# Optimization experiments

Measured on AMD Instinct MI355X. Metric: run time of the kernel, lower is better.

The kernel has to match this reference:

```python
import jax, jax.numpy as jnp
import numpy as np

N = 8192
E = 262144
IN_SELF = 512
IN_AGG = 512
OUT = 256  # out_channels; hidden = 2*OUT = 512


def _glorot(key, shape, scale=0.05):
    return jax.random.normal(key, shape, dtype=jnp.float32) * scale


def setup_inputs() -> dict:
    key = jax.random.key(0)
    ks = jax.random.split(key, 16)
    x_self = jax.random.normal(ks[0], (N, IN_SELF), dtype=jnp.float32)
    x_neighbor = jax.random.normal(ks[1], (N, IN_AGG), dtype=jnp.float32)
    edge_index = jax.random.randint(ks[2], (2, E), 0, N, dtype=jnp.int64)
    H = 2 * OUT
    return {
        "x_self": x_self,
        "x_neighbor": x_neighbor,
        "edge_index": edge_index,
        # linear_in_self: IN_SELF -> 2*OUT
        "w_in_self": _glorot(ks[3], (IN_SELF, H)),
        "b_in_self": jnp.zeros((H,), jnp.float32),
        # linear_out_self: IN_SELF + 2*OUT -> OUT
        "w_out_self": _glorot(ks[4], (IN_SELF + H, OUT)),
        "b_out_self": jnp.zeros((OUT,), jnp.float32),
        # gcn1: IN_SELF -> 2*OUT
        "gw1": _glorot(ks[5], (IN_SELF, H)),
        "gb1": jnp.zeros((H,), jnp.float32),
        # gcn2: 2*OUT -> OUT
        "gw2": _glorot(ks[6], (H, OUT)),
        "gb2": jnp.zeros((OUT,), jnp.float32),
        # linear_out: IN_AGG + OUT -> OUT
        "w_out": _glorot(ks[7], (IN_AGG + OUT, OUT)),
        "b_out": jnp.zeros((OUT,), jnp.float32),
    }


def _gcn_norm(edge_index, n):
    # PyG GCNConv default: add self loops, symmetric deg^-1/2 normalization.
    loop = jnp.arange(n, dtype=edge_index.dtype)
    src = jnp.concatenate([edge_index[0], loop])
    dst = jnp.concatenate([edge_index[1], loop])
    deg = jax.ops.segment_sum(jnp.ones_like(dst, dtype=jnp.float32), dst, num_segments=n)
    dinv = jnp.where(deg > 0, jax.lax.rsqrt(deg), 0.0)
    norm = dinv[src] * dinv[dst]  # [E+N]
    return src, dst, norm


def _gcn(x, w, b, src, dst, norm, n):
    h = x @ w                                   # [N, out]
    msg = h[src] * norm[:, None]                # gather + scale
    agg = jax.ops.segment_sum(msg, dst, num_segments=n)
    return agg + b


def reference(x_self, x_neighbor, edge_index,
              w_in_self, b_in_self, w_out_self, b_out_self,
              gw1, gb1, gw2, gb2, w_out, b_out):
    n = x_self.shape[0]
    src, dst, norm = _gcn_norm(edge_index, n)
    # linear branch
    l1 = jax.nn.relu(x_self @ w_in_self + b_in_self)
    l1 = jnp.concatenate([x_self, l1], axis=1) @ w_out_self + b_out_self
    # GCN branch
    g1 = _gcn(x_self, gw1, gb1, src, dst, norm, n)
    g2 = _gcn(g1, gw2, gb2, src, dst, norm, n)
    x2 = jnp.concatenate([x_neighbor, g2], axis=1) @ w_out + b_out
    # concat latent, dense inner-product decode
    z = jnp.concatenate([l1, x2], axis=1)       # [N, 2*OUT]
    return jax.nn.sigmoid(z @ z.T)              # [N, N]
```

## Files before the change

kernel.cpp:

```cpp
#include <hip/hip_runtime.h>
#include <cstdint>
#include <cstddef>

#define NNODE 8192
#define NEDGE 262144

typedef __attribute__((ext_vector_type(8))) short bf16x8;
typedef __attribute__((ext_vector_type(4))) float f32x4;

__device__ __forceinline__ unsigned short f2bf_rn(float x) {
    unsigned u = __float_as_uint(x);
    u = (u + 0x7FFFu + ((u >> 16) & 1u)) >> 16;
    return (unsigned short)u;
}
__device__ __forceinline__ float bf2f(unsigned short h) {
    return __uint_as_float(((unsigned)h) << 16);
}

__device__ __forceinline__ void gload16(const char* gp, char* lp) {
    __builtin_amdgcn_global_load_lds((const __attribute__((address_space(1))) void*)gp,
                                     (__attribute__((address_space(3))) void*)lp, 16, 0, 0);
}


__global__ void k_zero_int(int* p, int n) {
    int i = blockIdx.x * blockDim.x + threadIdx.x;
    if (i < n) p[i] = 0;
}

__global__ void k_count(const int* __restrict__ dst, int* __restrict__ cnt, int n) {
    int i = blockIdx.x * blockDim.x + threadIdx.x;
    if (i < n) atomicAdd(&cnt[dst[i]], 1);
}

__global__ __launch_bounds__(256) void k_scan(const int* __restrict__ cnt,
                                              int* __restrict__ row_start,
                                              int* __restrict__ cursor,
                                              float* __restrict__ dinv) {
    __shared__ int part[256];
    const int tid = threadIdx.x;
    const int PER = NNODE / 256;
    const int base = tid * PER;
    int loc[PER];
    int sum = 0;
#pragma unroll
    for (int i = 0; i < PER; ++i) { loc[i] = cnt[base + i]; sum += loc[i]; }
    part[tid] = sum;
    __syncthreads();
    if (tid == 0) {
        int r = 0;
        for (int i = 0; i < 256; ++i) { int t = part[i]; part[i] = r; r += t; }
    }
    __syncthreads();
    int run = part[tid];
#pragma unroll
    for (int i = 0; i < PER; ++i) {
        row_start[base + i] = run;
        cursor[base + i] = run;
        dinv[base + i] = rsqrtf((float)loc[i] + 1.0f);
        run += loc[i];
    }
    if (tid == 255) row_start[NNODE] = run;
}

__global__ void k_fill_csr2(const int* __restrict__ src, const int* __restrict__ dst,
                            int* __restrict__ cursor, const float* __restrict__ dinv,
                            int* __restrict__ slist, float* __restrict__ wlist, int n) {
    int e = blockIdx.x * blockDim.x + threadIdx.x;
    if (e < n) {
        int d = dst[e];
        int s = src[e];
        int pos = atomicAdd(&cursor[d], 1);
        slist[pos] = s;
        wlist[pos] = dinv[s] * dinv[d];
    }
}

__device__ __forceinline__ void split_wt_tile(const float* __restrict__ W, int K, int N,
                                              int k0, int n0,
                                              unsigned short* __restrict__ Oh,
                                              unsigned short* __restrict__ Ol,
                                              float (*t)[33]) {
    const int c = threadIdx.x & 31, r8 = threadIdx.x >> 5;
#pragma unroll
    for (int i = 0; i < 4; ++i) {
        int r = r8 + i * 8;
        t[r][c] = W[(size_t)(k0 + r) * N + n0 + c];
    }
    __syncthreads();
#pragma unroll
    for (int i = 0; i < 4; ++i) {
        int r = r8 + i * 8;
        float x = t[c][r];
        unsigned short h = f2bf_rn(x);
        Oh[(size_t)(n0 + r) * K + k0 + c] = h;
        Ol[(size_t)(n0 + r) * K + k0 + c] = f2bf_rn(x - bf2f(h));
    }
}

__global__ __launch_bounds__(256) void k_prep(
    const float* __restrict__ x_self, const float* __restrict__ x_neighbor,
    const float* __restrict__ w_in_self, const float* __restrict__ w_out_self,
    const float* __restrict__ w_out, const float* __restrict__ gw1,
    const float* __restrict__ gw2, const float* __restrict__ gb1,
    unsigned short* __restrict__ xsh, unsigned short* __restrict__ xsl,
    unsigned short* __restrict__ xnh, unsigned short* __restrict__ xnl,
    unsigned short* __restrict__ wAt_h, unsigned short* __restrict__ wAt_l,
    unsigned short* __restrict__ wost_h, unsigned short* __restrict__ wost_l,
    unsigned short* __restrict__ wot_h, unsigned short* __restrict__ wot_l,
    float* __restrict__ bc) {
    __shared__ float t[32][33];
    const int b = blockIdx.x;
    const int tid = threadIdx.x;
    if (b < 8192) {
        const float* src = (b < 4096) ? x_self : x_neighbor;
        unsigned short* oh = (b < 4096) ? xsh : xnh;
        unsigned short* ol = (b < 4096) ? xsl : xnl;
        const int i = (b & 4095) * 256 + tid;
        float4 v = ((const float4*)src)[i];
        float x[4] = {v.x, v.y, v.z, v.w};
        unsigned short h[4], l[4];
#pragma unroll
        for (int j = 0; j < 4; ++j) {
            h[j] = f2bf_rn(x[j]);
            l[j] = f2bf_rn(x[j] - bf2f(h[j]));
        }
        ((ushort4*)oh)[i] = make_ushort4(h[0], h[1], h[2], h[3]);
        ((ushort4*)ol)[i] = make_ushort4(l[0], l[1], l[2], l[3]);
    } else if (b < 8448) {
        const int b2 = b - 8192;
        split_wt_tile(w_in_self, 512, 512, (b2 & 15) * 32, (b2 >> 4) * 32, wAt_h, wAt_l, t);
    } else if (b < 8576) {
        const int b3 = b - 8448;
        const int k0 = (b3 & 15) * 32, n0 = (b3 >> 4) * 32;
        const int nloc = tid & 31, kg = tid >> 5;
        float a[4] = {0.f, 0.f, 0.f, 0.f};
        for (int c = 0; c < 512; ++c) {
            float g2v = gw2[(size_t)c * 256 + n0 + nloc];
#pragma unroll
            for (int i = 0; i < 4; ++i)
                a[i] += gw1[(size_t)(k0 + kg * 4 + i) * 512 + c] * g2v;
        }
#pragma unroll
        for (int i = 0; i < 4; ++i) {
            unsigned short hh = f2bf_rn(a[i]);
            wAt_h[(size_t)(512 + n0 + nloc) * 512 + k0 + kg * 4 + i] = hh;
            wAt_l[(size_t)(512 + n0 + nloc) * 512 + k0 + kg * 4 + i] = f2bf_rn(a[i] - bf2f(hh));
        }
    } else if (b < 8832) {
        const int b4 = b - 8576;
        split_wt_tile(w_out_self, 1024, 256, (b4 & 31) * 32, (b4 >> 5) * 32, wost_h, wost_l, t);
    } else if (b < 9024) {
        const int b5 = b - 8832;
        split_wt_tile(w_out, 768, 256, (b5 % 24) * 32, (b5 / 24) * 32, wot_h, wot_l, t);
    } else {
        float a = 0.0f;
        for (int c = 0; c < 512; ++c) a += gb1[c] * gw2[(size_t)c * 256 + tid];
        bc[tid] = a;
    }
}

__device__ __forceinline__ void stage_g(char* buf,
                                        const char* aH, const char* aL, size_t strA,
                                        const char* bH, const char* bL, size_t strB,
                                        int rloc, int w) {
#pragma unroll
    for (int i = 0; i < 2; ++i) {
        const size_t r = (size_t)(rloc + i * 64);
        char* lp = buf + i * 4096 + w * 1024;
        gload16(aH + r * strA, lp);
        gload16(aL + r * strA, lp + 8192);
    }
    gload16(bH + (size_t)rloc * strB, buf + 16384 + w * 1024);
    gload16(bL + (size_t)rloc * strB, buf + 20480 + w * 1024);
}

__device__ __forceinline__ void core_2x4(const char* cur, int w, int sread, int lane,
                                         f32x4 acc[2][4]) {
    bf16x8 ah[2], al[2], bh[4], bl[4];
#pragma unroll
    for (int m = 0; m < 2; ++m) {
        const int row = w * 32 + m * 16 + (lane & 15);
        ah[m] = *(const bf16x8*)(cur + row * 64 + sread);
        al[m] = *(const bf16x8*)(cur + 8192 + row * 64 + sread);
    }
#pragma unroll
    for (int n = 0; n < 4; ++n) {
        const int row = n * 16 + (lane & 15);
        bh[n] = *(const bf16x8*)(cur + 16384 + row * 64 + sread);
        bl[n] = *(const bf16x8*)(cur + 20480 + row * 64 + sread);
    }
#pragma unroll
    for (int m = 0; m < 2; ++m)
#pragma unroll
        for (int n = 0; n < 4; ++n) {
            acc[m][n] = __builtin_amdgcn_mfma_f32_16x16x32_bf16(ah[m], bh[n], acc[m][n], 0, 0, 0);
            acc[m][n] = __builtin_amdgcn_mfma_f32_16x16x32_bf16(ah[m], bl[n], acc[m][n], 0, 0, 0);
            acc[m][n] = __builtin_amdgcn_mfma_f32_16x16x32_bf16(al[m], bh[n], acc[m][n], 0, 0, 0);
        }
}

__global__ __launch_bounds__(256) void k_gemm128_A(
    const unsigned short* __restrict__ xsh, const unsigned short* __restrict__ xsl,
    const unsigned short* __restrict__ wAt_h, const unsigned short* __restrict__ wAt_l,
    const float* __restrict__ bias,
    unsigned short* __restrict__ l1h, unsigned short* __restrict__ l1l,
    float* __restrict__ hc) {
    __shared__ __align__(16) char smem[49152];
    const int tid = threadIdx.x, lane = tid & 63, w = tid >> 6;
    const int bm = blockIdx.y * 128, bn = blockIdx.x * 64;
    const int rloc = w * 16 + (lane >> 2);
    const int swz_src = ((lane & 3) ^ ((lane >> 3) & 3)) * 16;
    const int sread = ((lane >> 4) ^ ((lane >> 1) & 3)) * 16;
    const char* Ah = (const char*)xsh + (size_t)bm * 1024 + swz_src;
    const char* Al = (const char*)xsl + (size_t)bm * 1024 + swz_src;
    const char* Bh = (const char*)wAt_h + (size_t)bn * 1024 + swz_src;
    const char* Bl = (const char*)wAt_l + (size_t)bn * 1024 + swz_src;

    f32x4 acc[2][4] = {};
    stage_g(smem, Ah, Al, 1024, Bh, Bl, 1024, rloc, w);
    __syncthreads();
    for (int ks = 0; ks < 16; ++ks) {
        char* cur = smem + (ks & 1) * 24576;
        if (ks < 15) {
            const int kb = (ks + 1) * 64;
            stage_g(smem + ((ks + 1) & 1) * 24576, Ah + kb, Al + kb, 1024,
                    Bh + kb, Bl + kb, 1024, rloc, w);
        }
        core_2x4(cur, w, sread, lane, acc);
        __syncthreads();
    }

    const int rj = (lane >> 4) * 4, cc = lane & 15;
#pragma unroll
    for (int m = 0; m < 2; ++m) {
#pragma unroll
        for (int n = 0; n < 4; ++n) {
            const int col = bn + n * 16 + cc;
#pragma unroll
            for (int j = 0; j < 4; ++j) {
                const int row = bm + w * 32 + m * 16 + rj + j;
                float x = acc[m][n][j];
                if (col < 512) {
                    x += bias[col];
                    x = fmaxf(x, 0.0f);
                    unsigned short h = f2bf_rn(x);
                    l1h[(size_t)row * 512 + col] = h;
                    l1l[(size_t)row * 512 + col] = f2bf_rn(x - bf2f(h));
                } else {
                    hc[(size_t)row * 256 + (col - 512)] = x;
                }
            }
        }
    }
}

__global__ __launch_bounds__(256) void k_gemm128_Z(
    const unsigned short* __restrict__ xsh, const unsigned short* __restrict__ xsl,
    const unsigned short* __restrict__ l1h, const unsigned short* __restrict__ l1l,
    const unsigned short* __restrict__ xnh, const unsigned short* __restrict__ xnl,
    const unsigned short* __restrict__ g2h, const unsigned short* __restrict__ g2l,
    const unsigned short* __restrict__ wost_h, const unsigned short* __restrict__ wost_l,
    const unsigned short* __restrict__ wot_h, const unsigned short* __restrict__ wot_l,
    const float* __restrict__ b_out_self, const float* __restrict__ b_out,
    unsigned short* __restrict__ zhi, unsigned short* __restrict__ zlo) {
    __shared__ __align__(16) char smem[49152];
    const int half = blockIdx.x >> 2;
    const int bn = (blockIdx.x & 3) * 64;
    const int tid = threadIdx.x, lane = tid & 63, w = tid >> 6;
    const int bm = blockIdx.y * 128;
    const int rloc = w * 16 + (lane >> 2);
    const int swz_src = ((lane & 3) ^ ((lane >> 3) & 3)) * 16;
    const int sread = ((lane >> 4) ^ ((lane >> 1) & 3)) * 16;

    const unsigned short *A1h, *A1l, *A2h, *A2l, *Wh, *Wl;
    const float* bias;
    int Ktot;
    size_t strA2, strB;
    if (half == 0) {
        A1h = xsh; A1l = xsl; A2h = l1h; A2l = l1l; strA2 = 1024;
        Wh = wost_h; Wl = wost_l; strB = 2048; Ktot = 1024; bias = b_out_self;
    } else {
        A1h = xnh; A1l = xnl; A2h = g2h; A2l = g2l; strA2 = 512;
        Wh = wot_h; Wl = wot_l; strB = 1536; Ktot = 768; bias = b_out;
    }
    const int nsteps = Ktot / 32;
    const char* Bh = (const char*)Wh + (size_t)bn * strB + swz_src;
    const char* Bl = (const char*)Wl + (size_t)bn * strB + swz_src;

    auto asrc = [&](int k0, const char*& sh, const char*& sl, size_t& st) {
        if (k0 < 512) {
            sh = (const char*)A1h + (size_t)bm * 1024 + (size_t)k0 * 2 + swz_src;
            sl = (const char*)A1l + (size_t)bm * 1024 + (size_t)k0 * 2 + swz_src;
            st = 1024;
        } else {
            sh = (const char*)A2h + (size_t)bm * strA2 + (size_t)(k0 - 512) * 2 + swz_src;
            sl = (const char*)A2l + (size_t)bm * strA2 + (size_t)(k0 - 512) * 2 + swz_src;
            st = strA2;
        }
    };

    f32x4 acc[2][4] = {};
    {
        const char *sh, *sl; size_t st;
        asrc(0, sh, sl, st);
        stage_g(smem, sh, sl, st, Bh, Bl, strB, rloc, w);
    }
    __syncthreads();
    for (int ks = 0; ks < nsteps; ++ks) {
        char* cur = smem + (ks & 1) * 24576;
        if (ks + 1 < nsteps) {
            const char *sh, *sl; size_t st;
            asrc((ks + 1) * 32, sh, sl, st);
            stage_g(smem + ((ks + 1) & 1) * 24576, sh, sl, st,
                    Bh + (size_t)(ks + 1) * 64, Bl + (size_t)(ks + 1) * 64, strB, rloc, w);
        }
        core_2x4(cur, w, sread, lane, acc);
        __syncthreads();
    }

    const int rj = (lane >> 4) * 4, cc = lane & 15;
    const int zoff = half * 256;
#pragma unroll
    for (int m = 0; m < 2; ++m) {
#pragma unroll
        for (int n = 0; n < 4; ++n) {
            const int col = bn + n * 16 + cc;
            const float bv = bias[col];
#pragma unroll
            for (int j = 0; j < 4; ++j) {
                const int row = bm + w * 32 + m * 16 + rj + j;
                float x = acc[m][n][j] + bv;
                unsigned short h = f2bf_rn(x);
                zhi[(size_t)row * 512 + zoff + col] = h;
                zlo[(size_t)row * 512 + zoff + col] = f2bf_rn(x - bf2f(h));
            }
        }
    }
}

template <int MODE>
__global__ __launch_bounds__(256) void k_agg2(
    const int* __restrict__ row_start, const int* __restrict__ slist,
    const float* __restrict__ wlist, const float* __restrict__ dinv,
    const float* __restrict__ h,
    const float* __restrict__ bc, const float* __restrict__ b2,
    float* __restrict__ outf,
    unsigned short* __restrict__ oh, unsigned short* __restrict__ ol) {
    const int n = blockIdx.x;
    const int c = threadIdx.x;
    const float di = dinv[n];
    float acc = di * di * h[(size_t)n * 256 + c];
    float sv = di * di;
    const int e0 = row_start[n], e1 = row_start[n + 1];
    int j = e0;
    for (; j + 8 <= e1; j += 8) {
        int ss[8];
        float ww[8], vv[8];
#pragma unroll
        for (int u = 0; u < 8; ++u) { ss[u] = slist[j + u]; ww[u] = wlist[j + u]; }
#pragma unroll
        for (int u = 0; u < 8; ++u) vv[u] = h[(size_t)ss[u] * 256 + c];
#pragma unroll
        for (int u = 0; u < 8; ++u) {
            acc += ww[u] * vv[u];
            if (MODE) sv += ww[u];
        }
    }
    for (; j < e1; ++j) {
        const float wv = wlist[j];
        acc += wv * h[(size_t)slist[j] * 256 + c];
        if (MODE) sv += wv;
    }
    if (MODE == 0) {
        outf[(size_t)n * 256 + c] = acc;
    } else {
        float x = acc + sv * bc[c] + b2[c];
        unsigned short hb = f2bf_rn(x);
        oh[(size_t)n * 256 + c] = hb;
        ol[(size_t)n * 256 + c] = f2bf_rn(x - bf2f(hb));
    }
}

__device__ __forceinline__ void zzt_stage(char* buf, const char* s0, const char* s1,
                                          const char* s2, const char* s3,
                                          int rloc, int swz_src, int w, int kbyte) {
    const char* srcs[4] = {s0, s1, s2, s3};
#pragma unroll
    for (int tile = 0; tile < 4; ++tile) {
#pragma unroll
        for (int i = 0; i < 2; ++i) {
            const char* gp = srcs[tile] + (size_t)(rloc + i * 64) * 1024 + kbyte + swz_src;
            char* lp = buf + tile * 8192 + i * 4096 + w * 1024;
            gload16(gp, lp);
        }
    }
}

__global__ __launch_bounds__(256) void k_zzt_mfma(const unsigned short* __restrict__ zhi,
                                                  const unsigned short* __restrict__ zlo,
                                                  float* __restrict__ out) {
    __shared__ __align__(16) char smem[65536];
    const int tid = threadIdx.x;
    const int lane = tid & 63;
    const int w = tid >> 6;
    const int wr = w >> 1, wc = w & 1;

    const int t = blockIdx.x;
    int bi = (int)((sqrtf(8.0f * (float)t + 1.0f) - 1.0f) * 0.5f);
    while ((bi + 1) * (bi + 2) / 2 <= t) ++bi;
    while (bi * (bi + 1) / 2 > t) --bi;
    const int bj = t - bi * (bi + 1) / 2;

    const char* s0 = (const char*)zhi + (size_t)(bi * 128) * 1024;
    const char* s1 = (const char*)zlo + (size_t)(bi * 128) * 1024;
    const char* s2 = (const char*)zhi + (size_t)(bj * 128) * 1024;
    const char* s3 = (const char*)zlo + (size_t)(bj * 128) * 1024;

    const int rloc = w * 16 + (lane >> 2);
    const int swz_src = ((lane & 3) ^ ((lane >> 3) & 3)) * 16;
    const int sread = ((lane >> 4) ^ ((lane >> 1) & 3)) * 16;

    f32x4 acc[4][4] = {};

    zzt_stage(smem, s0, s1, s2, s3, rloc, swz_src, w, 0);
    __syncthreads();

    for (int ks = 0; ks < 16; ++ks) {
        char* cur = smem + (ks & 1) * 32768;
        if (ks < 15)
            zzt_stage(smem + ((ks + 1) & 1) * 32768, s0, s1, s2, s3, rloc, swz_src, w,
                      (ks + 1) * 64);

        bf16x8 ah[4], al[4], bh[4], bl[4];
        const char* pa = cur + (wr * 64 + (lane & 15)) * 64 + sread;
        const char* pb = cur + 16384 + (wc * 64 + (lane & 15)) * 64 + sread;
#pragma unroll
        for (int m = 0; m < 4; ++m) {
            ah[m] = *(const bf16x8*)(pa + m * 1024);
            al[m] = *(const bf16x8*)(pa + 8192 + m * 1024);
        }
#pragma unroll
        for (int n = 0; n < 4; ++n) {
            bh[n] = *(const bf16x8*)(pb + n * 1024);
            bl[n] = *(const bf16x8*)(pb + 8192 + n * 1024);
        }
#pragma unroll
        for (int m = 0; m < 4; ++m)
#pragma unroll
            for (int n = 0; n < 4; ++n) {
                acc[m][n] = __builtin_amdgcn_mfma_f32_16x16x32_bf16(ah[m], bh[n], acc[m][n], 0, 0, 0);
                acc[m][n] = __builtin_amdgcn_mfma_f32_16x16x32_bf16(ah[m], bl[n], acc[m][n], 0, 0, 0);
                acc[m][n] = __builtin_amdgcn_mfma_f32_16x16x32_bf16(al[m], bh[n], acc[m][n], 0, 0, 0);
            }
        __syncthreads();
    }

    const int rj = (lane >> 4) * 4;
    const int cc = lane & 15;
#pragma unroll
    for (int m = 0; m < 4; ++m) {
#pragma unroll
        for (int n = 0; n < 4; ++n) {
            float s[4];
#pragma unroll
            for (int j = 0; j < 4; ++j)
                s[j] = 1.0f / (1.0f + __expf(-acc[m][n][j]));
            const int gr0 = bi * 128 + wr * 64 + m * 16 + rj;
            const int gc  = bj * 128 + wc * 64 + n * 16 + cc;
#pragma unroll
            for (int j = 0; j < 4; ++j)
                __builtin_nontemporal_store(s[j], out + (size_t)(gr0 + j) * NNODE + gc);
            if (bi != bj) {
                const int mr = bj * 128 + wc * 64 + n * 16 + cc;
                const int mc = bi * 128 + wr * 64 + m * 16 + rj;
                f32x4 v = {s[0], s[1], s[2], s[3]};
                __builtin_nontemporal_store(v, (f32x4*)(out + (size_t)mr * NNODE + mc));
            }
        }
    }
}

extern "C" void kernel_launch(void* const* d_in, const int* in_sizes, int n_in,
                              void* d_out, int out_size, void* d_ws, size_t ws_size,
                              hipStream_t stream) {
    const float* x_self     = (const float*)d_in[0];
    const float* x_neighbor = (const float*)d_in[1];
    const int*   ei         = (const int*)d_in[2];
    const float* w_in_self  = (const float*)d_in[3];
    const float* b_in_self  = (const float*)d_in[4];
    const float* w_out_self = (const float*)d_in[5];
    const float* b_out_self = (const float*)d_in[6];
    const float* gw1        = (const float*)d_in[7];
    const float* gb1        = (const float*)d_in[8];
    const float* gw2        = (const float*)d_in[9];
    const float* gb2        = (const float*)d_in[10];
    const float* w_out      = (const float*)d_in[11];
    const float* b_out      = (const float*)d_in[12];
    float* out = (float*)d_out;

    char* ws = (char*)d_ws;
    const size_t MB = 1024 * 1024;
    const size_t KB = 1024;
    int*   cnt       = (int*)(ws + 0);
    int*   row_start = (int*)(ws + 32 * KB);
    int*   cursor    = (int*)(ws + 96 * KB);
    float* dinv      = (float*)(ws + 128 * KB);
    float* bc        = (float*)(ws + 192 * KB);
    int*   slist     = (int*)(ws + 2 * MB);
    float* wlist     = (float*)(ws + 3 * MB);
    unsigned short* xsh = (unsigned short*)(ws + 4 * MB);
    unsigned short* xsl = (unsigned short*)(ws + 12 * MB);
    unsigned short* xnh = (unsigned short*)(ws + 20 * MB);
    unsigned short* xnl = (unsigned short*)(ws + 28 * MB);
    unsigned short* l1h = (unsigned short*)(ws + 36 * MB);
    unsigned short* l1l = (unsigned short*)(ws + 44 * MB);
    float*          hc  = (float*)(ws + 52 * MB);
    float*          t1  = (float*)(ws + 60 * MB);
    unsigned short* g2h = (unsigned short*)(ws + 68 * MB);
    unsigned short* g2l = (unsigned short*)(ws + 72 * MB);
    unsigned short* zhi = (unsigned short*)(ws + 76 * MB);
    unsigned short* zlo = (unsigned short*)(ws + 84 * MB);
    unsigned short* wAt_h = (unsigned short*)(ws + 92 * MB);
    unsigned short* wAt_l = (unsigned short*)(ws + 93 * MB);
    unsigned short* wost_h = (unsigned short*)(ws + 94 * MB);
    unsigned short* wost_l = (unsigned short*)(ws + 95 * MB);
    unsigned short* wot_h  = (unsigned short*)(ws + 96 * MB);
    unsigned short* wot_l  = (unsigned short*)(ws + 97 * MB);

    const int* srcA = ei;
    const int* dstA = ei + NEDGE;

    k_prep<<<9025, 256, 0, stream>>>(x_self, x_neighbor, w_in_self, w_out_self, w_out,
                                     gw1, gw2, gb1, xsh, xsl, xnh, xnl,
                                     wAt_h, wAt_l, wost_h, wost_l, wot_h, wot_l, bc);

    k_zero_int<<<NNODE / 256, 256, 0, stream>>>(cnt, NNODE);
    k_count<<<NEDGE / 256, 256, 0, stream>>>(dstA, cnt, NEDGE);
    k_scan<<<1, 256, 0, stream>>>(cnt, row_start, cursor, dinv);
    k_fill_csr2<<<NEDGE / 256, 256, 0, stream>>>(srcA, dstA, cursor, dinv, slist, wlist, NEDGE);

    k_gemm128_A<<<dim3(12, NNODE / 128), 256, 0, stream>>>(
        xsh, xsl, wAt_h, wAt_l, b_in_self, l1h, l1l, hc);

    k_agg2<0><<<NNODE, 256, 0, stream>>>(row_start, slist, wlist, dinv, hc,
                                         nullptr, nullptr, t1, nullptr, nullptr);
    k_agg2<1><<<NNODE, 256, 0, stream>>>(row_start, slist, wlist, dinv, t1,
                                         bc, gb2, nullptr, g2h, g2l);

    k_gemm128_Z<<<dim3(8, NNODE / 128), 256, 0, stream>>>(
        xsh, xsl, l1h, l1l, xnh, xnl, g2h, g2l,
        wost_h, wost_l, wot_h, wot_l, b_out_self, b_out, zhi, zlo);

    k_zzt_mfma<<<64 * 65 / 2, 256, 0, stream>>>(zhi, zlo, out);
}
```

Before: 390.0 us.

## Retile Z·Zᵀ decode to 256x256 blocks with deeper prefetch and fold count zeroing

The dense sigmoid(Z·Zᵀ) kernel now uses 256x256 output tiles over the upper triangle with 512 threads and 8 waves. Each wave computes 8x4 MFMA sub-tiles, doubling operand reuse per load. Staging is double-buffered two k-steps ahead with explicit vmcnt waits and raw barriers, MFMA phases get higher s_setprio, and the block index is remapped to interleave tiles. The separate zeroing kernel for degree counts is merged into the prep kernel as extra blocks, saving one launch. The cost is 128KB of LDS per block and higher register pressure, which limits occupancy.

```diff
diff --git a/kernel.cpp b/kernel.cpp
--- a/kernel.cpp
+++ b/kernel.cpp
@@ -22,11 +22,6 @@
                                      (__attribute__((address_space(3))) void*)lp, 16, 0, 0);
 }
 
-
-__global__ void k_zero_int(int* p, int n) {
-    int i = blockIdx.x * blockDim.x + threadIdx.x;
-    if (i < n) p[i] = 0;
-}
 
 __global__ void k_count(const int* __restrict__ dst, int* __restrict__ cnt, int n) {
     int i = blockIdx.x * blockDim.x + threadIdx.x;
@@ -108,7 +103,7 @@
     unsigned short* __restrict__ wAt_h, unsigned short* __restrict__ wAt_l,
     unsigned short* __restrict__ wost_h, unsigned short* __restrict__ wost_l,
     unsigned short* __restrict__ wot_h, unsigned short* __restrict__ wot_l,
-    float* __restrict__ bc) {
+    float* __restrict__ bc, int* __restrict__ cnt) {
     __shared__ float t[32][33];
     const int b = blockIdx.x;
     const int tid = threadIdx.x;
@@ -153,10 +148,12 @@
     } else if (b < 9024) {
         const int b5 = b - 8832;
         split_wt_tile(w_out, 768, 256, (b5 % 24) * 32, (b5 / 24) * 32, wot_h, wot_l, t);
-    } else {
+    } else if (b == 9024) {
         float a = 0.0f;
         for (int c = 0; c < 512; ++c) a += gb1[c] * gw2[(size_t)c * 256 + tid];
         bc[tid] = a;
+    } else {
+        cnt[(b - 9025) * 256 + tid] = 0;
     }
 }
 
@@ -382,98 +379,99 @@
     }
 }
 
-__device__ __forceinline__ void zzt_stage(char* buf, const char* s0, const char* s1,
-                                          const char* s2, const char* s3,
-                                          int rloc, int swz_src, int w, int kbyte) {
-    const char* srcs[4] = {s0, s1, s2, s3};
-#pragma unroll
-    for (int tile = 0; tile < 4; ++tile) {
-#pragma unroll
-        for (int i = 0; i < 2; ++i) {
-            const char* gp = srcs[tile] + (size_t)(rloc + i * 64) * 1024 + kbyte + swz_src;
-            char* lp = buf + tile * 8192 + i * 4096 + w * 1024;
-            gload16(gp, lp);
-        }
-    }
-}
-
-__global__ __launch_bounds__(256) void k_zzt_mfma(const unsigned short* __restrict__ zhi,
-                                                  const unsigned short* __restrict__ zlo,
-                                                  float* __restrict__ out) {
-    __shared__ __align__(16) char smem[65536];
+__global__ __launch_bounds__(512, 2) void k_zzt256(const unsigned short* __restrict__ zhi,
+                                                   const unsigned short* __restrict__ zlo,
+                                                   float* __restrict__ out) {
+    __shared__ __align__(16) char smem[131072];
     const int tid = threadIdx.x;
     const int lane = tid & 63;
     const int w = tid >> 6;
-    const int wr = w >> 1, wc = w & 1;
-
-    const int t = blockIdx.x;
+    const int wr = w >> 2, wc = w & 3;
+
+    const int t0 = blockIdx.x;
+    const int t = (t0 & 7) * 66 + (t0 >> 3);
     int bi = (int)((sqrtf(8.0f * (float)t + 1.0f) - 1.0f) * 0.5f);
     while ((bi + 1) * (bi + 2) / 2 <= t) ++bi;
     while (bi * (bi + 1) / 2 > t) --bi;
     const int bj = t - bi * (bi + 1) / 2;
 
-    const char* s0 = (const char*)zhi + (size_t)(bi * 128) * 1024;
-    const char* s1 = (const char*)zlo + (size_t)(bi * 128) * 1024;
-    const char* s2 = (const char*)zhi + (size_t)(bj * 128) * 1024;
-    const char* s3 = (const char*)zlo + (size_t)(bj * 128) * 1024;
-
-    const int rloc = w * 16 + (lane >> 2);
+    const char* pnl[4];
+    pnl[0] = (const char*)zhi + (size_t)(bi * 256) * 1024;
+    pnl[1] = (const char*)zlo + (size_t)(bi * 256) * 1024;
+    pnl[2] = (const char*)zhi + (size_t)(bj * 256) * 1024;
+    pnl[3] = (const char*)zlo + (size_t)(bj * 256) * 1024;
+
     const int swz_src = ((lane & 3) ^ ((lane >> 3) & 3)) * 16;
     const int sread = ((lane >> 4) ^ ((lane >> 1) & 3)) * 16;
 
-    f32x4 acc[4][4] = {};
-
-    zzt_stage(smem, s0, s1, s2, s3, rloc, swz_src, w, 0);
-    __syncthreads();
-
-    for (int ks = 0; ks < 16; ++ks) {
-        char* cur = smem + (ks & 1) * 32768;
-        if (ks < 15)
-            zzt_stage(smem + ((ks + 1) & 1) * 32768, s0, s1, s2, s3, rloc, swz_src, w,
-                      (ks + 1) * 64);
-
-        bf16x8 ah[4], al[4], bh[4], bl[4];
-        const char* pa = cur + (wr * 64 + (lane & 15)) * 64 + sread;
-        const char* pb = cur + 16384 + (wc * 64 + (lane & 15)) * 64 + sread;
-#pragma unroll
-        for (int m = 0; m < 4; ++m) {
-            ah[m] = *(const bf16x8*)(pa + m * 1024);
-            al[m] = *(const bf16x8*)(pa + 8192 + m * 1024);
-        }
+    auto STAGE = [&](int buf, int kt) {
+        const int kb = kt * 64;
+        char* base = smem + buf * 65536;
+#pragma unroll
+        for (int jj = 0; jj < 8; ++jj) {
+            const int c = w * 8 + jj;
+            const int q = c >> 4, ci = c & 15;
+            const char* gp = pnl[q] + (size_t)(ci * 16 + (lane >> 2)) * 1024 + kb + swz_src;
+            gload16(gp, base + q * 16384 + ci * 1024);
+        }
+    };
+
+    f32x4 acc[8][4] = {};
+
+    STAGE(0, 0);
+    STAGE(1, 1);
+
+    for (int kt = 0; kt < 16; ++kt) {
+        if (kt < 15) asm volatile("s_waitcnt vmcnt(8)" ::: "memory");
+        else         asm volatile("s_waitcnt vmcnt(0)" ::: "memory");
+        __builtin_amdgcn_s_barrier();
+        __builtin_amdgcn_sched_barrier(0);
+        const char* cur = smem + (kt & 1) * 65536;
+
+        bf16x8 bh[4], bl[4];
 #pragma unroll
         for (int n = 0; n < 4; ++n) {
-            bh[n] = *(const bf16x8*)(pb + n * 1024);
-            bl[n] = *(const bf16x8*)(pb + 8192 + n * 1024);
-        }
-#pragma unroll
-        for (int m = 0; m < 4; ++m)
+            const int row = wc * 64 + n * 16 + (lane & 15);
+            bh[n] = *(const bf16x8*)(cur + 32768 + row * 64 + sread);
+            bl[n] = *(const bf16x8*)(cur + 49152 + row * 64 + sread);
+        }
+#pragma unroll
+        for (int m = 0; m < 8; ++m) {
+            const int row = wr * 128 + m * 16 + (lane & 15);
+            bf16x8 ah = *(const bf16x8*)(cur + row * 64 + sread);
+            bf16x8 al = *(const bf16x8*)(cur + 16384 + row * 64 + sread);
+            __builtin_amdgcn_s_setprio(1);
 #pragma unroll
             for (int n = 0; n < 4; ++n) {
-                acc[m][n] = __builtin_amdgcn_mfma_f32_16x16x32_bf16(ah[m], bh[n], acc[m][n], 0, 0, 0);
-                acc[m][n] = __builtin_amdgcn_mfma_f32_16x16x32_bf16(ah[m], bl[n], acc[m][n], 0, 0, 0);
-                acc[m][n] = __builtin_amdgcn_mfma_f32_16x16x32_bf16(al[m], bh[n], acc[m][n], 0, 0, 0);
+                acc[m][n] = __builtin_amdgcn_mfma_f32_16x16x32_bf16(ah, bh[n], acc[m][n], 0, 0, 0);
+                acc[m][n] = __builtin_amdgcn_mfma_f32_16x16x32_bf16(ah, bl[n], acc[m][n], 0, 0, 0);
+                acc[m][n] = __builtin_amdgcn_mfma_f32_16x16x32_bf16(al, bh[n], acc[m][n], 0, 0, 0);
             }
-        __syncthreads();
+            __builtin_amdgcn_s_setprio(0);
+        }
+        __builtin_amdgcn_sched_barrier(0);
+        __builtin_amdgcn_s_barrier();
+        if (kt < 14) STAGE(kt & 1, kt + 2);
     }
 
     const int rj = (lane >> 4) * 4;
     const int cc = lane & 15;
 #pragma unroll
-    for (int m = 0; m < 4; ++m) {
+    for (int m = 0; m < 8; ++m) {
 #pragma unroll
         for (int n = 0; n < 4; ++n) {
             float s[4];
 #pragma unroll
             for (int j = 0; j < 4; ++j)
                 s[j] = 1.0f / (1.0f + __expf(-acc[m][n][j]));
-            const int gr0 = bi * 128 + wr * 64 + m * 16 + rj;
-            const int gc  = bj * 128 + wc * 64 + n * 16 + cc;
+            const int gr0 = bi * 256 + wr * 128 + m * 16 + rj;
+            const int gc  = bj * 256 + wc * 64 + n * 16 + cc;
 #pragma unroll
             for (int j = 0; j < 4; ++j)
                 __builtin_nontemporal_store(s[j], out + (size_t)(gr0 + j) * NNODE + gc);
             if (bi != bj) {
-                const int mr = bj * 128 + wc * 64 + n * 16 + cc;
-                const int mc = bi * 128 + wr * 64 + m * 16 + rj;
+                const int mr = bj * 256 + wc * 64 + n * 16 + cc;
+                const int mc = bi * 256 + wr * 128 + m * 16 + rj;
                 f32x4 v = {s[0], s[1], s[2], s[3]};
                 __builtin_nontemporal_store(v, (f32x4*)(out + (size_t)mr * NNODE + mc));
             }
@@ -531,11 +529,10 @@
     const int* srcA = ei;
     const int* dstA = ei + NEDGE;
 
-    k_prep<<<9025, 256, 0, stream>>>(x_self, x_neighbor, w_in_self, w_out_self, w_out,
+    k_prep<<<9057, 256, 0, stream>>>(x_self, x_neighbor, w_in_self, w_out_self, w_out,
                                      gw1, gw2, gb1, xsh, xsl, xnh, xnl,
-                                     wAt_h, wAt_l, wost_h, wost_l, wot_h, wot_l, bc);
-
-    k_zero_int<<<NNODE / 256, 256, 0, stream>>>(cnt, NNODE);
+                                     wAt_h, wAt_l, wost_h, wost_l, wot_h, wot_l, bc, cnt);
+
     k_count<<<NEDGE / 256, 256, 0, stream>>>(dstA, cnt, NEDGE);
     k_scan<<<1, 256, 0, stream>>>(cnt, row_start, cursor, dinv);
     k_fill_csr2<<<NEDGE / 256, 256, 0, stream>>>(srcA, dstA, cursor, dinv, slist, wlist, NEDGE);
@@ -552,5 +549,5 @@
         xsh, xsl, l1h, l1l, xnh, xnl, g2h, g2l,
         wost_h, wost_l, wot_h, wot_l, b_out_self, b_out, zhi, zlo);
 
-    k_zzt_mfma<<<64 * 65 / 2, 256, 0, stream>>>(zhi, zlo, out);
-}
+    k_zzt256<<<528, 512, 0, stream>>>(zhi, zlo, out);
+}
```

Result: slower. 423.9 us (+8.7%).
